# Optimization experiments

Measured on AMD Instinct MI355X. Metric: run time of the kernel, lower is better.

The kernel has to match this reference:

```python
import jax, jax.numpy as jnp
import numpy as np


def _grid_edges(hh, ww):
    """Directed 4-neighbor grid edges over an hh x ww patch grid, plus self-loops
    (PyG gcn_norm adds self-loops with weight 1)."""
    idx = np.arange(hh * ww).reshape(hh, ww)
    src = np.concatenate([idx[1:].ravel(), idx[:-1].ravel(), idx[:, 1:].ravel(), idx[:, :-1].ravel()])
    dst = np.concatenate([idx[:-1].ravel(), idx[1:].ravel(), idx[:, :-1].ravel(), idx[:, 1:].ravel()])
    loops = np.arange(hh * ww)
    return np.concatenate([src, loops]), np.concatenate([dst, loops])


def setup_inputs() -> dict:
    key = jax.random.key(0)
    k1, k2, k3, k4 = jax.random.split(key, 4)
    B, C, H, W = 4, 3, 512, 512
    E = 192
    p = 2
    x = jax.random.normal(k1, (B, C, H, W), dtype=jnp.float32)
    conv_w = jax.random.normal(k2, (E, C, p, p), dtype=jnp.float32) * (1.0 / np.sqrt(C * p * p))
    gcn_w = jax.random.normal(k3, (E, E), dtype=jnp.float32) * (1.0 / np.sqrt(E))
    gcn_b = jax.random.normal(k4, (E,), dtype=jnp.float32) * 0.02
    return {"x": x, "conv_w": conv_w, "gcn_w": gcn_w, "gcn_b": gcn_b}


def reference(x, conv_w, gcn_w, gcn_b):
    B, C, H, W = x.shape
    E, _, p, _ = conv_w.shape
    hh, ww = H // p, W // p
    N = hh * ww

    # Conv2d(kernel=stride=p, bias=False) == patchify + linear projection.
    xr = x.reshape(B, C, hh, p, ww, p)
    feats = jnp.einsum('bciujv,ecuv->bije', xr, conv_w).reshape(B, N, E)  # [B, N, E]

    # Grid graph (shared across batch), with self-loops.
    src_np, dst_np = _grid_edges(hh, ww)
    src = jnp.asarray(src_np, dtype=jnp.int32)
    dst = jnp.asarray(dst_np, dtype=jnp.int32)

    # GCNConv: out = D^{-1/2} (A + I) D^{-1/2} (X W^T) + b
    deg = jax.ops.segment_sum(jnp.ones(src.shape[0], feats.dtype), dst, num_segments=N)
    dinv = jax.lax.rsqrt(deg)  # deg >= 1 due to self-loops
    norm = dinv[src] * dinv[dst]  # [Etot]

    xw = jnp.einsum('bnc,oc->bno', feats, gcn_w)  # linear (PyG stores W as [out, in])
    msgs = xw[:, src, :] * norm[None, :, None]  # gather + scale: [B, Etot, E]
    agg = jax.vmap(lambda m: jax.ops.segment_sum(m, dst, num_segments=N))(msgs)  # scatter-sum
    return agg + gcn_b  # [B, N, E]
```

## Files before the change

kernel.cpp:

```cpp
#include <hip/hip_runtime.h>
#include <cstddef>

constexpr int kH  = 512, kW = 512, kC = 3;
constexpr int kHH = 256, kWW = 256;
constexpr int kN  = kHH * kWW;
constexpr int kE  = 192, kK = 12, kB = 4;

typedef float nt_f4 __attribute__((ext_vector_type(4)));

__device__ __forceinline__ float dinvf(int i, int j) {
    int deg = 1 + (i > 0) + (i < kHH - 1) + (j > 0) + (j < kWW - 1);
    return rsqrtf((float)deg);
}

__global__ __launch_bounds__(64) void build_M(const float* __restrict__ gcn_w,
                                              const float* __restrict__ conv_w,
                                              float* __restrict__ M) {
    const int e = blockIdx.x;
    const int lane = threadIdx.x;
    float acc[kK];
#pragma unroll
    for (int k = 0; k < kK; ++k) acc[k] = 0.f;
    for (int j = lane; j < kE; j += 64) {
        const float g = gcn_w[e * kE + j];
        const float4 c0 = *(const float4*)(conv_w + j * kK + 0);
        const float4 c1 = *(const float4*)(conv_w + j * kK + 4);
        const float4 c2 = *(const float4*)(conv_w + j * kK + 8);
        acc[0] += g * c0.x; acc[1] += g * c0.y; acc[2]  += g * c0.z; acc[3]  += g * c0.w;
        acc[4] += g * c1.x; acc[5] += g * c1.y; acc[6]  += g * c1.z; acc[7]  += g * c1.w;
        acc[8] += g * c2.x; acc[9] += g * c2.y; acc[10] += g * c2.z; acc[11] += g * c2.w;
    }
#pragma unroll
    for (int k = 0; k < kK; ++k) {
        float v = acc[k];
#pragma unroll
        for (int off = 32; off > 0; off >>= 1) v += __shfl_down(v, off);
        if (lane == 0) M[e * kK + k] = v;
    }
}

constexpr int THREADS = 192;
constexpr int ROWPAD  = 516;

__global__ __launch_bounds__(THREADS) void fused_gcn(
        const float* __restrict__ x, const float* __restrict__ M,
        const float* __restrict__ bias, float* __restrict__ out) {
    __shared__ float s_x[kC][6][ROWPAD];
    __shared__ float s_aggp[kWW][kK];

    const int t = threadIdx.x;
    const int i = blockIdx.x % kHH;
    const int b = blockIdx.x / kHH;

    const int e4  = t % 48;
    const int sub = t / 48;
    const int e   = e4 * 4;
    float4 mrow[12];
#pragma unroll
    for (int r = 0; r < 12; ++r) mrow[r] = ((const float4*)(M + (size_t)e * kK))[r];
    const float4 bv = *(const float4*)(bias + e);

    const int r0 = 2 * i - 2;
#pragma unroll
    for (int q = 0; q < 12; ++q) {
        const int idx  = t + q * THREADS;
        const int cr   = idx >> 7;
        const int col4 = idx & 127;
        const int c = cr / 6, row = cr % 6;
        const int rg = r0 + row;
        float4 val = make_float4(0.f, 0.f, 0.f, 0.f);
        if (rg >= 0 && rg < kH)
            val = *(const float4*)(x + (((size_t)(b * kC + c) * kH + rg) * kW) + col4 * 4);
        *(float4*)&s_x[c][row][col4 * 4] = val;
    }
    __syncthreads();

#pragma unroll
    for (int q = 0; q < 16; ++q) {
        const int idx = t + q * THREADS;
        const int j   = idx / kK;
        const int k   = idx % kK;
        const int c = k >> 2, u = (k >> 1) & 1, v = k & 1;
        const int col = 2 * j + v;
        const float dc = dinvf(i, j);
        const float du = dinvf(i - 1, j);
        const float dd = dinvf(i + 1, j);
        float sum = dc * s_x[c][u + 2][col]
                  + du * s_x[c][u][col]
                  + dd * s_x[c][u + 4][col];
        if (j > 0)       sum += dinvf(i, j - 1) * s_x[c][u + 2][col - 2];
        if (j < kWW - 1) sum += dinvf(i, j + 1) * s_x[c][u + 2][col + 2];
        s_aggp[j][k] = dc * sum;
    }
    __syncthreads();

    float* outb = out + ((size_t)b * kN + (size_t)i * kWW) * kE + e;
#pragma unroll 4
    for (int it = 0; it < kWW / 4; ++it) {
        const int nl = it * 4 + sub;
        const float4 a0 = *((const float4*)&s_aggp[nl][0]);
        const float4 a1 = *((const float4*)&s_aggp[nl][4]);
        const float4 a2 = *((const float4*)&s_aggp[nl][8]);
        nt_f4 acc;
#pragma unroll
        for (int r = 0; r < 4; ++r) {
            const float4 m0 = mrow[r * 3 + 0];
            const float4 m1 = mrow[r * 3 + 1];
            const float4 m2 = mrow[r * 3 + 2];
            float s = ((const float*)&bv)[r];
            s += m0.x * a0.x + m0.y * a0.y + m0.z * a0.z + m0.w * a0.w;
            s += m1.x * a1.x + m1.y * a1.y + m1.z * a1.z + m1.w * a1.w;
            s += m2.x * a2.x + m2.y * a2.y + m2.z * a2.z + m2.w * a2.w;
            acc[r] = s;
        }
        __builtin_nontemporal_store(acc, (nt_f4*)(outb + (size_t)nl * kE));
    }
}

extern "C" void kernel_launch(void* const* d_in, const int* in_sizes, int n_in,
                              void* d_out, int out_size, void* d_ws, size_t ws_size,
                              hipStream_t stream) {
    const float* x      = (const float*)d_in[0];
    const float* conv_w = (const float*)d_in[1];
    const float* gcn_w  = (const float*)d_in[2];
    const float* gcn_b  = (const float*)d_in[3];
    float* out = (float*)d_out;
    float* M   = (float*)d_ws;

    build_M<<<kE, 64, 0, stream>>>(gcn_w, conv_w, M);
    fused_gcn<<<kB * kHH, THREADS, 0, stream>>>(x, M, gcn_b, out);
}
```

Baseline: 232.3 us.

## Add patchify prepass, split rows into half-width blocks, swizzle block order

Adds a separate patchify kernel that writes the input as node-major 12-float patch vectors into workspace. The main kernel then reads neighbor patches directly (up/down from global, left/right from a small shared tile) instead of staging six input rows in LDS. Each block now covers half a row, which doubles the grid and shrinks shared memory, and block IDs are remapped across 8 groups. The rsqrt is replaced by a lookup of constants. The cost is an extra kernel launch and an extra round-trip of the input through global memory.

```diff
diff --git a/kernel.cpp b/kernel.cpp
--- a/kernel.cpp
+++ b/kernel.cpp
@@ -9,8 +9,11 @@
 typedef float nt_f4 __attribute__((ext_vector_type(4)));
 
 __device__ __forceinline__ float dinvf(int i, int j) {
-    int deg = 1 + (i > 0) + (i < kHH - 1) + (j > 0) + (j < kWW - 1);
-    return rsqrtf((float)deg);
+    const int deg = 1 + (i > 0) + (i < kHH - 1) + (j > 0) + (j < kWW - 1);
+    float r = 0.44721359549995794f;
+    if (deg == 4) r = 0.5f;
+    if (deg == 3) r = 0.5773502691896258f;
+    return r;
 }
 
 __global__ __launch_bounds__(64) void build_M(const float* __restrict__ gcn_w,
@@ -39,18 +42,43 @@
     }
 }
 
+__global__ __launch_bounds__(256) void patchify(const float* __restrict__ x,
+                                                float* __restrict__ P) {
+    const int i = blockIdx.x & (kHH - 1);
+    const int b = blockIdx.x >> 8;
+    const int j = threadIdx.x;
+    float p[12];
+#pragma unroll
+    for (int c = 0; c < kC; ++c)
+#pragma unroll
+        for (int u = 0; u < 2; ++u) {
+            const float2 t2 = *(const float2*)(x + ((size_t)(b * kC + c) * kH + (2 * i + u)) * kW + 2 * j);
+            p[c * 4 + u * 2 + 0] = t2.x;
+            p[c * 4 + u * 2 + 1] = t2.y;
+        }
+    float* dst = P + ((size_t)(b * kHH + i) * kWW + j) * kK;
+    *(float4*)(dst + 0) = make_float4(p[0], p[1], p[2],  p[3]);
+    *(float4*)(dst + 4) = make_float4(p[4], p[5], p[6],  p[7]);
+    *(float4*)(dst + 8) = make_float4(p[8], p[9], p[10], p[11]);
+}
+
 constexpr int THREADS = 192;
-constexpr int ROWPAD  = 516;
+constexpr int JB      = 128;
 
-__global__ __launch_bounds__(THREADS) void fused_gcn(
-        const float* __restrict__ x, const float* __restrict__ M,
+__global__ __launch_bounds__(THREADS, 4) void fused_gcn(
+        const float* __restrict__ P, const float* __restrict__ M,
         const float* __restrict__ bias, float* __restrict__ out) {
-    __shared__ float s_x[kC][6][ROWPAD];
-    __shared__ float s_aggp[kWW][kK];
+    __shared__ float s_P[(JB + 2) * kK];
+    __shared__ float s_agg[JB][kK];
 
     const int t = threadIdx.x;
-    const int i = blockIdx.x % kHH;
-    const int b = blockIdx.x / kHH;
+
+    const int bid  = (int)blockIdx.x;
+    const int wg   = (bid & 7) * 256 + (bid >> 3);
+    const int half = wg & 1;
+    const int i    = (wg >> 1) & (kHH - 1);
+    const int b    = wg >> 9;
+    const int j0   = half * JB;
 
     const int e4  = t % 48;
     const int sub = t / 48;
@@ -60,47 +88,52 @@
     for (int r = 0; r < 12; ++r) mrow[r] = ((const float4*)(M + (size_t)e * kK))[r];
     const float4 bv = *(const float4*)(bias + e);
 
-    const int r0 = 2 * i - 2;
+    const float* Prow = P + ((long long)(b * kHH + i) * kWW + (j0 - 1)) * kK;
 #pragma unroll
-    for (int q = 0; q < 12; ++q) {
-        const int idx  = t + q * THREADS;
-        const int cr   = idx >> 7;
-        const int col4 = idx & 127;
-        const int c = cr / 6, row = cr % 6;
-        const int rg = r0 + row;
-        float4 val = make_float4(0.f, 0.f, 0.f, 0.f);
-        if (rg >= 0 && rg < kH)
-            val = *(const float4*)(x + (((size_t)(b * kC + c) * kH + rg) * kW) + col4 * 4);
-        *(float4*)&s_x[c][row][col4 * 4] = val;
+    for (int q = 0; q < 3; ++q) {
+        const int f4 = t + q * THREADS;
+        if (f4 < 3 * (JB + 2)) {
+            const int node = f4 / 3;
+            const int jg   = j0 - 1 + node;
+            float4 v = make_float4(0.f, 0.f, 0.f, 0.f);
+            if (jg >= 0 && jg < kWW)
+                v = *(const float4*)(Prow + (long long)f4 * 4);
+            *(float4*)(&s_P[f4 * 4]) = v;
+        }
     }
     __syncthreads();
 
+    const float* Pu = P + ((long long)(b * kHH + (i - 1)) * kWW + j0) * kK;
+    const float* Pd = P + ((long long)(b * kHH + (i + 1)) * kWW + j0) * kK;
 #pragma unroll
-    for (int q = 0; q < 16; ++q) {
+    for (int q = 0; q < 8; ++q) {
         const int idx = t + q * THREADS;
         const int j   = idx / kK;
-        const int k   = idx % kK;
-        const int c = k >> 2, u = (k >> 1) & 1, v = k & 1;
-        const int col = 2 * j + v;
-        const float dc = dinvf(i, j);
-        const float du = dinvf(i - 1, j);
-        const float dd = dinvf(i + 1, j);
-        float sum = dc * s_x[c][u + 2][col]
-                  + du * s_x[c][u][col]
-                  + dd * s_x[c][u + 4][col];
-        if (j > 0)       sum += dinvf(i, j - 1) * s_x[c][u + 2][col - 2];
-        if (j < kWW - 1) sum += dinvf(i, j + 1) * s_x[c][u + 2][col + 2];
-        s_aggp[j][k] = dc * sum;
+        const int k   = idx - j * kK;
+        const int jg  = j0 + j;
+        const float pc = s_P[(j + 1) * kK + k];
+        const float pl = s_P[ j      * kK + k];
+        const float pr = s_P[(j + 2) * kK + k];
+        float pu = 0.f, pd = 0.f;
+        if (i > 0)       pu = Pu[idx];
+        if (i < kHH - 1) pd = Pd[idx];
+        const float dc = dinvf(i, jg);
+        float s = dc * pc;
+        s += dinvf(i - 1, jg) * pu;
+        s += dinvf(i + 1, jg) * pd;
+        s += dinvf(i, jg - 1) * pl;
+        s += dinvf(i, jg + 1) * pr;
+        s_agg[j][k] = dc * s;
     }
     __syncthreads();
 
-    float* outb = out + ((size_t)b * kN + (size_t)i * kWW) * kE + e;
+    float* outb = out + ((size_t)b * kN + (size_t)i * kWW + j0) * kE + e;
 #pragma unroll 4
-    for (int it = 0; it < kWW / 4; ++it) {
+    for (int it = 0; it < JB / 4; ++it) {
         const int nl = it * 4 + sub;
-        const float4 a0 = *((const float4*)&s_aggp[nl][0]);
-        const float4 a1 = *((const float4*)&s_aggp[nl][4]);
-        const float4 a2 = *((const float4*)&s_aggp[nl][8]);
+        const float4 a0 = *((const float4*)&s_agg[nl][0]);
+        const float4 a1 = *((const float4*)&s_agg[nl][4]);
+        const float4 a2 = *((const float4*)&s_agg[nl][8]);
         nt_f4 acc;
 #pragma unroll
         for (int r = 0; r < 4; ++r) {
@@ -126,7 +159,9 @@
     const float* gcn_b  = (const float*)d_in[3];
     float* out = (float*)d_out;
     float* M   = (float*)d_ws;
+    float* P   = (float*)d_ws + 2304;
 
     build_M<<<kE, 64, 0, stream>>>(gcn_w, conv_w, M);
-    fused_gcn<<<kB * kHH, THREADS, 0, stream>>>(x, M, gcn_b, out);
+    patchify<<<kB * kHH, 256, 0, stream>>>(x, P);
+    fused_gcn<<<kB * kHH * 2, THREADS, 0, stream>>>(P, M, gcn_b, out);
 }
```

Result: no change. 235.9 us (+1.5%).
